# Kernel tuning notes

Measured on AMD Instinct MI355X. Metric: run time of the kernel, lower is better.

The kernel has to match this reference:

```python
import jax, jax.numpy as jnp
import numpy as np

B, N, D, H = 4, 2048, 1024, 16
HD = D // H
LR_SCALE = 0.01  # base step size for the fast-weight test-time update
EPS = 1e-6


def setup_inputs() -> dict:
    key = jax.random.key(0)
    ks = jax.random.split(key, 11)
    s = 0.02
    x = jax.random.normal(ks[0], (B, N, D), jnp.float32)
    Wq = jax.random.normal(ks[1], (D, D), jnp.float32) * s
    Wk = jax.random.normal(ks[2], (D, D), jnp.float32) * s
    Wv = jax.random.normal(ks[3], (D, D), jnp.float32) * s
    Wo = jax.random.normal(ks[4], (D, D), jnp.float32) * s
    w1_init = jax.random.normal(ks[5], (H, HD, HD), jnp.float32) * s  # FastWeightGLU init state
    w3_init = jax.random.normal(ks[6], (H, HD, HD), jnp.float32) * s
    W_lr = jax.random.normal(ks[7], (D, H), jnp.float32) * s  # FastWeightHpGLU lr head
    norm_w = jnp.ones((D,), jnp.float32)  # grouped RMSNorm weight
    Wg1 = jax.random.normal(ks[8], (D, HD), jnp.float32) * s  # output_gate bottleneck
    Wg2 = jax.random.normal(ks[9], (HD, D), jnp.float32) * s
    return dict(x=x, Wq=Wq, Wk=Wk, Wv=Wv, Wo=Wo, w1_init=w1_init,
                w3_init=w3_init, W_lr=W_lr, norm_w=norm_w, Wg1=Wg1, Wg2=Wg2)


def _fast_weight_train(q, k, v, lr, w1_init, w3_init):
    # q,k,v: (b,n,h,hd); lr: (b,n,h); fast weight f(x) = silu(x@W1) * (x@W3)
    b = q.shape[0]
    W1_0 = jnp.broadcast_to(w1_init, (b,) + w1_init.shape)
    W3_0 = jnp.broadcast_to(w3_init, (b,) + w3_init.shape)

    def step(carry, inp):
        W1, W3 = carry
        q_t, k_t, v_t, lr_t = inp  # (b,h,hd), lr_t: (b,h,1)
        h1 = jnp.einsum('bhd,bhde->bhe', k_t, W1)
        h3 = jnp.einsum('bhd,bhde->bhe', k_t, W3)
        sg = jax.nn.sigmoid(h1)
        s1 = h1 * sg  # silu(h1)
        err = s1 * h3 - v_t  # d(0.5||f(k)-v||^2)/df
        dsilu = sg * (1.0 + h1 * (1.0 - sg))
        g1 = err * h3 * dsilu
        g3 = err * s1
        W1 = W1 - lr_t[..., None] * jnp.einsum('bhd,bhe->bhde', k_t, g1)
        W3 = W3 - lr_t[..., None] * jnp.einsum('bhd,bhe->bhde', k_t, g3)
        o1 = jnp.einsum('bhd,bhde->bhe', q_t, W1)
        o3 = jnp.einsum('bhd,bhde->bhe', q_t, W3)
        return (W1, W3), jax.nn.silu(o1) * o3

    xs = (q.transpose(1, 0, 2, 3), k.transpose(1, 0, 2, 3),
          v.transpose(1, 0, 2, 3), lr.transpose(1, 0, 2)[..., None])
    (W1, W3), outs = jax.lax.scan(step, (W1_0, W3_0), xs)
    return outs.transpose(1, 0, 2, 3), (W1, W3)  # (b,n,h,hd)


def reference(x, Wq, Wk, Wv, Wo, w1_init, w3_init, W_lr, norm_w, Wg1, Wg2):
    b, n, d = x.shape
    h = w1_init.shape[0]
    hd = d // h
    q = jax.nn.silu((x @ Wq).reshape(b, n, h, hd))
    k = jax.nn.silu((x @ Wk).reshape(b, n, h, hd))
    v = (x @ Wv).reshape(b, n, h, hd)
    lr = LR_SCALE * jax.nn.sigmoid(x @ W_lr)  # (b,n,h) per-token hyper-param
    out, _ = _fast_weight_train(q, k, v, lr, w1_init, w3_init)
    # grouped RMSNorm (per head) fused with sigmoid output gate
    rms = jax.lax.rsqrt(jnp.mean(out * out, axis=-1, keepdims=True) + EPS)
    out = (out * rms).reshape(b, n, d) * norm_w
    gate = (x @ Wg1) @ Wg2
    out = out * jax.nn.sigmoid(gate)
    return out @ Wo
```

## Files before the change

### kernel.cpp

```cpp
#include <hip/hip_runtime.h>
#include <hip/hip_bf16.h>

#define B_ 4
#define N_ 2048
#define D_ 1024
#define H_ 16
#define HD_ 64
#define MTOT (B_*N_)
#define CH_ 16
#define NCH_ (N_/CH_)

typedef __attribute__((ext_vector_type(8))) short short8v;
typedef __attribute__((ext_vector_type(4))) float f32x4;

__device__ __forceinline__ float fsig(float x){
  return __builtin_amdgcn_rcpf(1.0f + __expf(-x));
}

__global__ void k_cast_bf16(const float* __restrict__ in, __hip_bfloat16* __restrict__ out, int n4){
  int i = blockIdx.x*256 + threadIdx.x;
  if (i >= n4) return;
  float4 vv = ((const float4*)in)[i];
  __hip_bfloat16 b0 = __float2bfloat16(vv.x), b1 = __float2bfloat16(vv.y),
                 b2 = __float2bfloat16(vv.z), b3 = __float2bfloat16(vv.w);
  ushort4 o;
  o.x = *(const unsigned short*)&b0; o.y = *(const unsigned short*)&b1;
  o.z = *(const unsigned short*)&b2; o.w = *(const unsigned short*)&b3;
  ((ushort4*)out)[i] = o;
}

__global__ void k_transpose_cast(const float* __restrict__ in, __hip_bfloat16* __restrict__ out,
                                 int R, int C){
  __shared__ float tile[64][65];
  int r0 = blockIdx.y*64, c0 = blockIdx.x*64;
  int tid = threadIdx.x;
  #pragma unroll
  for (int i=0;i<16;i++){ int idx = tid + i*256; int rr = idx>>6, cc = idx&63;
    tile[rr][cc] = in[(size_t)(r0+rr)*C + (c0+cc)]; }
  __syncthreads();
  #pragma unroll
  for (int i=0;i<16;i++){ int idx = tid + i*256; int rr = idx>>6, cc = idx&63;
    out[(size_t)(c0+rr)*R + (r0+cc)] = __float2bfloat16(tile[cc][rr]); }
}

__global__ void k_prep_wgl(const float* __restrict__ Wg1, const float* __restrict__ Wlr,
                           __hip_bfloat16* __restrict__ WgL){
  int idx = blockIdx.x*256 + threadIdx.x;
  int r = idx >> 10, d = idx & 1023;
  float v = 0.f;
  if (r < 64) v = Wg1[(size_t)d*64 + r];
  else if (r < 80) v = Wlr[(size_t)d*16 + (r-64)];
  WgL[idx] = __float2bfloat16(v);
}

__global__ void k_post_gl(const float* __restrict__ proj, __hip_bfloat16* __restrict__ t1,
                          float* __restrict__ lrout){
  int m = blockIdx.x*4 + (threadIdx.x>>6);
  int e = threadIdx.x & 63;
  float val = proj[(size_t)m*128 + e];
  t1[(size_t)m*64 + e] = __float2bfloat16(val);
  if (e < 16){
    float s = proj[(size_t)m*128 + 64 + e];
    lrout[(size_t)m*16 + e] = 0.01f*fsig(s);
  }
}

__device__ __forceinline__ void gl2lds16(const void* g, void* l){
  __builtin_amdgcn_global_load_lds((const __attribute__((address_space(1))) void*)g,
                                   (__attribute__((address_space(3))) void*)l, 16, 0, 0);
}

template<int ACT, int LAYOUT>
__global__ __launch_bounds__(256,2) void k_gemm_bt2(
    const __hip_bfloat16* __restrict__ A, const __hip_bfloat16* __restrict__ BT,
    float* __restrict__ C, int M, int N, int K)
{
  __shared__ short As[128*32];
  __shared__ short Bs[128*32];
  const int n0 = blockIdx.x*128, m0 = blockIdx.y*128;
  const int tid = threadIdx.x, lane = tid & 63, wid = tid >> 6;
  const int wm = wid >> 1, wn = wid & 1;
  const short* Aps = (const short*)A;
  const short* Bps = (const short*)BT;
  f32x4 acc[4][4] = {};
  const int srow = wid*32 + (lane>>2);
  const int scol = (lane&3)*8;
  const size_t aoff0 = (size_t)(m0+srow)*K + scol;
  const size_t boff0 = (size_t)(n0+srow)*K + scol;
  short* lA = As + wid*1024;
  short* lB = Bs + wid*1024;
  const int row = lane & 15, kq = (lane >> 4)*8;
  for (int kk = 0; kk < K; kk += 32) {
    __syncthreads();
    gl2lds16(Aps + aoff0 + kk,                 lA);
    gl2lds16(Aps + aoff0 + (size_t)16*K + kk,  lA + 512);
    gl2lds16(Bps + boff0 + kk,                 lB);
    gl2lds16(Bps + boff0 + (size_t)16*K + kk,  lB + 512);
    __syncthreads();
    short8v af[4], bfr[4];
    #pragma unroll
    for (int i=0;i<4;i++) af[i]  = *(const short8v*)(As + (wm*64 + i*16 + row)*32 + kq);
    #pragma unroll
    for (int j=0;j<4;j++) bfr[j] = *(const short8v*)(Bs + (wn*64 + j*16 + row)*32 + kq);
    #pragma unroll
    for (int i=0;i<4;i++)
      #pragma unroll
      for (int j=0;j<4;j++)
        acc[i][j] = __builtin_amdgcn_mfma_f32_16x16x32_bf16(af[i], bfr[j], acc[i][j], 0, 0, 0);
  }
  #pragma unroll
  for (int i=0;i<4;i++){
    #pragma unroll
    for (int j=0;j<4;j++){
      int col = n0 + wn*64 + j*16 + (lane & 15);
      #pragma unroll
      for (int qq=0; qq<4; ++qq){
        int rowg = m0 + wm*64 + i*16 + (lane>>4)*4 + qq;
        float val = acc[i][j][qq];
        if (ACT==1) val = val*fsig(val);
        if (LAYOUT==0) {
          C[(size_t)rowg*N + col] = val;
        } else {
          size_t oidx = ((((size_t)(rowg>>11))*16 + (col>>6))*(size_t)N_ + (size_t)(rowg & 2047))*64
                        + (size_t)(col & 63);
          C[oidx] = val;
        }
      }
    }
  }
}

__device__ __forceinline__ unsigned short bfr16(float x){
  __hip_bfloat16 b = __float2bfloat16(x);
  return *(unsigned short*)&b;
}
__device__ __forceinline__ short8v cvt_frag(const float4 a, const float4 c){
  short8v r;
  r[0]=(short)bfr16(a.x); r[1]=(short)bfr16(a.y); r[2]=(short)bfr16(a.z); r[3]=(short)bfr16(a.w);
  r[4]=(short)bfr16(c.x); r[5]=(short)bfr16(c.y); r[6]=(short)bfr16(c.z); r[7]=(short)bfr16(c.w);
  return r;
}

__global__ __launch_bounds__(256,1) void k_scan8(
    const float* __restrict__ q, const float* __restrict__ k, const float* __restrict__ v,
    const float* __restrict__ lr, const float* __restrict__ w1i, const float* __restrict__ w3i,
    float* __restrict__ so)
{
  const int blk = blockIdx.x;
  const int bh  = blk >> 2;
  const int sl  = blk & 3;
  const int b = bh >> 4, h = bh & 15;
  const int e0 = sl*16;
  const int tid = threadIdx.x, lane = tid & 63, wid = tid >> 6;
  const int tA = lane & 15, ks8 = (lane >> 4)*8;

  __shared__ __align__(16) __hip_bfloat16 Wb1[16*64];
  __shared__ __align__(16) __hip_bfloat16 Wb3[16*64];
  __shared__ __align__(16) float KW1e[256], KW3e[256];
  __shared__ __align__(16) float QW1[256], QW3[256];
  __shared__ __align__(16) float GKK[256], GQK[256];
  __shared__ __align__(16) float C13[512];

  const int we = tid & 15;
  const int wd = (tid >> 4) * 4;
  float w1r[4], w3r[4];
  {
    const float* w1p = w1i + (size_t)h*HD_*HD_ + e0 + we;
    const float* w3p = w3i + (size_t)h*HD_*HD_ + e0 + we;
    #pragma unroll
    for (int j=0;j<4;j++){ w1r[j] = w1p[(size_t)(wd+j)*64]; w3r[j] = w3p[(size_t)(wd+j)*64]; }
  }
  const int mir_off = we*128 + ((wd*2) ^ ((we&7)<<4));
  auto write_mirrors = [&](){
    uint2 p1, p3;
    p1.x = (unsigned)bfr16(w1r[0]) | ((unsigned)bfr16(w1r[1])<<16);
    p1.y = (unsigned)bfr16(w1r[2]) | ((unsigned)bfr16(w1r[3])<<16);
    p3.x = (unsigned)bfr16(w3r[0]) | ((unsigned)bfr16(w3r[1])<<16);
    p3.y = (unsigned)bfr16(w3r[2]) | ((unsigned)bfr16(w3r[3])<<16);
    *(uint2*)((char*)Wb1 + mir_off) = p1;
    *(uint2*)((char*)Wb3 + mir_off) = p3;
  };
  write_mirrors();

  const float* kfb = k + (size_t)bh*N_*64;
  const float* qfb = q + (size_t)bh*N_*64;
  const float* vfb = v + (size_t)bh*N_*64;
  const float* lrp = lr + ((size_t)b*N_)*16 + h;
  float* sob = so + (((size_t)b*N_)*16 + h)*64 + e0;

  auto mir_read = [&](const __hip_bfloat16* Wm, int m)->short8v{
    return *(const short8v*)((const char*)Wm + tA*128 + (((m*32+ks8)*2) ^ ((tA&7)<<4)));
  };

  float4 fA0,fA1,fA2,fA3;
  float4 fB0,fB1,fB2,fB3;
  float  vvr[16], lrr[16];

  if (wid >= 1) {
    const float* xr = ((wid==2) ? qfb : kfb) + (size_t)tA*64;
    fA0 = *(const float4*)(xr+ks8);    fA1 = *(const float4*)(xr+ks8+4);
    fA2 = *(const float4*)(xr+32+ks8); fA3 = *(const float4*)(xr+32+ks8+4);
    if (wid==3){
      const float* qr = qfb + (size_t)tA*64;
      fB0 = *(const float4*)(qr+ks8);    fB1 = *(const float4*)(qr+ks8+4);
      fB2 = *(const float4*)(qr+32+ks8); fB3 = *(const float4*)(qr+32+ks8+4);
    }
  } else if (lane < 16) {
    #pragma unroll
    for (int t=0;t<CH_;++t){
      vvr[t] = vfb[(size_t)t*64 + e0 + lane];
      lrr[t] = lrp[(size_t)t*16];
    }
  }
  __syncthreads();

  #pragma unroll 1
  for (int c = 0; c < NCH_; ++c) {
    const int t0 = c*CH_;

    if (wid == 1) {
      short8v af0 = cvt_frag(fA0,fA1), af1 = cvt_frag(fA2,fA3);
      const int slot = (((lane>>4)*4) ^ ((( tA>>1)&3)<<2));
      f32x4 acc = {};
      acc = __builtin_amdgcn_mfma_f32_16x16x32_bf16(af0, mir_read(Wb1,0), acc, 0,0,0);
      acc = __builtin_amdgcn_mfma_f32_16x16x32_bf16(af1, mir_read(Wb1,1), acc, 0,0,0);
      *(f32x4*)&KW1e[tA*16 + slot] = acc;
      f32x4 ac3 = {};
      ac3 = __builtin_amdgcn_mfma_f32_16x16x32_bf16(af0, mir_read(Wb3,0), ac3, 0,0,0);
      ac3 = __builtin_amdgcn_mfma_f32_16x16x32_bf16(af1, mir_read(Wb3,1), ac3, 0,0,0);
      *(f32x4*)&KW3e[tA*16 + slot] = ac3;
    } else if (wid == 2) {
      short8v af0 = cvt_frag(fA0,fA1), af1 = cvt_frag(fA2,fA3);
      f32x4 acc = {};
      acc = __builtin_amdgcn_mfma_f32_16x16x32_bf16(af0, mir_read(Wb1,0), acc, 0,0,0);
      acc = __builtin_amdgcn_mfma_f32_16x16x32_bf16(af1, mir_read(Wb1,1), acc, 0,0,0);
      #pragma unroll
      for (int qq=0;qq<4;++qq) QW1[((lane>>4)*4+qq)*16 + tA] = acc[qq];
      f32x4 ac3 = {};
      ac3 = __builtin_amdgcn_mfma_f32_16x16x32_bf16(af0, mir_read(Wb3,0), ac3, 0,0,0);
      ac3 = __builtin_amdgcn_mfma_f32_16x16x32_bf16(af1, mir_read(Wb3,1), ac3, 0,0,0);
      #pragma unroll
      for (int qq=0;qq<4;++qq) QW3[((lane>>4)*4+qq)*16 + tA] = ac3[qq];
    } else if (wid == 3) {
      short8v af0 = cvt_frag(fA0,fA1), af1 = cvt_frag(fA2,fA3);
      short8v aq0 = cvt_frag(fB0,fB1), aq1 = cvt_frag(fB2,fB3);
      f32x4 acc = {};
      acc = __builtin_amdgcn_mfma_f32_16x16x32_bf16(af0, af0, acc, 0,0,0);
      acc = __builtin_amdgcn_mfma_f32_16x16x32_bf16(af1, af1, acc, 0,0,0);
      #pragma unroll
      for (int qq=0;qq<4;++qq) GKK[((lane>>4)*4+qq)*16 + tA] = acc[qq];
      f32x4 ac2 = {};
      ac2 = __builtin_amdgcn_mfma_f32_16x16x32_bf16(aq0, af0, ac2, 0,0,0);
      ac2 = __builtin_amdgcn_mfma_f32_16x16x32_bf16(aq1, af1, ac2, 0,0,0);
      #pragma unroll
      for (int qq=0;qq<4;++qq) GQK[((lane>>4)*4+qq)*16 + tA] = ac2[qq];
    }
    __syncthreads();

    const int tn0 = ((c+1 < NCH_) ? c+1 : c) * CH_;
    if (wid >= 1) {
      const float* xr = ((wid==2) ? qfb : kfb) + (size_t)(tn0+tA)*64;
      fA0 = *(const float4*)(xr+ks8);    fA1 = *(const float4*)(xr+ks8+4);
      fA2 = *(const float4*)(xr+32+ks8); fA3 = *(const float4*)(xr+32+ks8+4);
      if (wid==3){
        const float* qr = qfb + (size_t)(tn0+tA)*64;
        fB0 = *(const float4*)(qr+ks8);    fB1 = *(const float4*)(qr+ks8+4);
        fB2 = *(const float4*)(qr+32+ks8); fB3 = *(const float4*)(qr+32+ks8+4);
      }
    } else if (lane < 16) {
      float vvn[16], lrn[16];
      #pragma unroll
      for (int t=0;t<CH_;++t){
        vvn[t] = vfb[(size_t)(tn0+t)*64 + e0 + lane];
        lrn[t] = lrp[(size_t)(tn0+t)*16];
      }
      float a1[16], a3[16];
      const int swr = ((lane>>1)&3)<<2;
      #pragma unroll
      for (int i2=0;i2<4;i2++){
        f32x4 x1 = *(const f32x4*)&KW1e[lane*16 + ((i2*4) ^ swr)];
        f32x4 x3 = *(const f32x4*)&KW3e[lane*16 + ((i2*4) ^ swr)];
        a1[i2*4+0]=x1[0]; a1[i2*4+1]=x1[1]; a1[i2*4+2]=x1[2]; a1[i2*4+3]=x1[3];
        a3[i2*4+0]=x3[0]; a3[i2*4+1]=x3[1]; a3[i2*4+2]=x3[2]; a3[i2*4+3]=x3[3];
      }
      f32x4 grow[3][4];
      #pragma unroll
      for (int i2=0;i2<4;i2++){
        grow[0][i2] = *(const f32x4*)&GKK[ 0 + i2*4];
        grow[1][i2] = *(const f32x4*)&GKK[16 + i2*4];
        grow[2][i2] = *(const f32x4*)&GKK[32 + i2*4];
      }
      #pragma unroll
      for (int t = 0; t < CH_; ++t) {
        const float h1 = a1[t], h3 = a3[t];
        const float sg = fsig(h1);
        const float s1 = h1*sg;
        const float er = fmaf(s1, h3, -vvr[t]);
        const float ds = sg*fmaf(h1, 1.0f - sg, 1.0f);
        const float lt = lrr[t];
        float2 cc; cc.x = lt*(er*h3*ds); cc.y = lt*(er*s1);
        *(float2*)&C13[(t*16+lane)*2] = cc;
        #pragma unroll
        for (int t2 = t+1; t2 < CH_; ++t2) {
          const float g = grow[t%3][t2>>2][t2&3];
          a1[t2] = fmaf(-g, cc.x, a1[t2]);
          a3[t2] = fmaf(-g, cc.y, a3[t2]);
        }
        if (t + 3 < CH_) {
          #pragma unroll
          for (int i2=0;i2<4;i2++) grow[(t+3)%3][i2] = *(const f32x4*)&GKK[(t+3)*16 + i2*4];
        }
      }
      #pragma unroll
      for (int t=0;t<CH_;++t){ vvr[t]=vvn[t]; lrr[t]=lrn[t]; }
    }
    __syncthreads();

    {
      const int ot = tid >> 4, oe = tid & 15;
      float o1 = QW1[ot*16+oe], o3 = QW3[ot*16+oe];
      #pragma unroll
      for (int s = 0; s < CH_; ++s) {
        const float gl2 = GQK[ot*16+s];
        const float2 cc = *(const float2*)&C13[(s*16+oe)*2];
        const float g = (s <= ot) ? gl2 : 0.0f;
        o1 = fmaf(-g, cc.x, o1);
        o3 = fmaf(-g, cc.y, o3);
      }
      sob[(size_t)(t0+ot)*(H_*HD_) + oe] = (o1*fsig(o1))*o3;
    }

    #pragma unroll
    for (int s = 0; s < CH_; ++s) {
      const float2 cc = *(const float2*)&C13[(s*16+we)*2];
      const float4 ks = *(const float4*)(kfb + (size_t)(t0+s)*64 + wd);
      w1r[0] = fmaf(-ks.x, cc.x, w1r[0]); w1r[1] = fmaf(-ks.y, cc.x, w1r[1]);
      w1r[2] = fmaf(-ks.z, cc.x, w1r[2]); w1r[3] = fmaf(-ks.w, cc.x, w1r[3]);
      w3r[0] = fmaf(-ks.x, cc.y, w3r[0]); w3r[1] = fmaf(-ks.y, cc.y, w3r[1]);
      w3r[2] = fmaf(-ks.z, cc.y, w3r[2]); w3r[3] = fmaf(-ks.w, cc.y, w3r[3]);
    }
    write_mirrors();
    __syncthreads();
  }
}

__global__ void k_norm_gate(const float* __restrict__ so, const float* __restrict__ gate,
                            const float* __restrict__ nw, __hip_bfloat16* __restrict__ y)
{
  int idx = blockIdx.x*4 + (threadIdx.x>>6);
  int e = threadIdx.x & 63;
  float o = so[(size_t)idx*64 + e];
  float ss = o*o;
  #pragma unroll
  for (int m=32; m>=1; m>>=1) ss += __shfl_xor(ss, m, 64);
  float rms = rsqrtf(ss*(1.0f/64.0f) + 1e-6f);
  int hh = idx & 15;
  size_t bn = (size_t)(idx >> 4);
  int d = hh*64 + e;
  float g = gate[bn*1024 + d];
  float val = o*rms*nw[d] * fsig(g);
  y[bn*1024 + d] = __float2bfloat16(val);
}

extern "C" void kernel_launch(void* const* d_in, const int* in_sizes, int n_in,
                              void* d_out, int out_size, void* d_ws, size_t ws_size,
                              hipStream_t stream)
{
  const float* x   = (const float*)d_in[0];
  const float* Wq  = (const float*)d_in[1];
  const float* Wk  = (const float*)d_in[2];
  const float* Wv  = (const float*)d_in[3];
  const float* Wo  = (const float*)d_in[4];
  const float* w1i = (const float*)d_in[5];
  const float* w3i = (const float*)d_in[6];
  const float* Wlr = (const float*)d_in[7];
  const float* nw  = (const float*)d_in[8];
  const float* Wg1 = (const float*)d_in[9];
  const float* Wg2 = (const float*)d_in[10];
  float* out = (float*)d_out;

  char* p = (char*)d_ws;
  auto take = [&](size_t bytes)->void*{ void* r = (void*)p; p += (bytes + 255) & ~(size_t)255; return r; };
  __hip_bfloat16* xb   = (__hip_bfloat16*)take((size_t)MTOT*D_*2);
  __hip_bfloat16* Wqt  = (__hip_bfloat16*)take((size_t)D_*D_*2);
  __hip_bfloat16* Wkt  = (__hip_bfloat16*)take((size_t)D_*D_*2);
  __hip_bfloat16* Wvt  = (__hip_bfloat16*)take((size_t)D_*D_*2);
  __hip_bfloat16* Wot  = (__hip_bfloat16*)take((size_t)D_*D_*2);
  __hip_bfloat16* Wg2t = (__hip_bfloat16*)take((size_t)D_*HD_*2);
  __hip_bfloat16* WgL  = (__hip_bfloat16*)take((size_t)128*D_*2);
  __hip_bfloat16* t1b  = (__hip_bfloat16*)take((size_t)MTOT*HD_*2);
  float* projt = (float*)take((size_t)MTOT*128*4);
  float* qf  = (float*)take((size_t)MTOT*D_*4);
  float* kf  = (float*)take((size_t)MTOT*D_*4);
  float* vf  = (float*)take((size_t)MTOT*D_*4);
  float* lrb = (float*)take((size_t)MTOT*H_*4);
  float* sob = (float*)take((size_t)MTOT*D_*4);
  __hip_bfloat16* yb = (__hip_bfloat16*)take((size_t)MTOT*D_*2);

  k_cast_bf16<<<MTOT*D_/4/256, 256, 0, stream>>>(x, xb, MTOT*D_/4);
  k_transpose_cast<<<dim3(16,16), 256, 0, stream>>>(Wq, Wqt, D_, D_);
  k_transpose_cast<<<dim3(16,16), 256, 0, stream>>>(Wk, Wkt, D_, D_);
  k_transpose_cast<<<dim3(16,16), 256, 0, stream>>>(Wv, Wvt, D_, D_);
  k_transpose_cast<<<dim3(16,16), 256, 0, stream>>>(Wo, Wot, D_, D_);
  k_transpose_cast<<<dim3(16,1),  256, 0, stream>>>(Wg2, Wg2t, HD_, D_);
  k_prep_wgl<<<512, 256, 0, stream>>>(Wg1, Wlr, WgL);
  k_gemm_bt2<0,0><<<dim3(1,64), 256, 0, stream>>>(xb, WgL, projt, MTOT, 128, D_);
  k_post_gl<<<MTOT/4, 256, 0, stream>>>(projt, t1b, lrb);
  k_gemm_bt2<1,1><<<dim3(8,64), 256, 0, stream>>>(xb, Wqt, qf, MTOT, D_, D_);
  k_gemm_bt2<1,1><<<dim3(8,64), 256, 0, stream>>>(xb, Wkt, kf, MTOT, D_, D_);
  k_gemm_bt2<0,1><<<dim3(8,64), 256, 0, stream>>>(xb, Wvt, vf, MTOT, D_, D_);
  k_gemm_bt2<0,0><<<dim3(8,64), 256, 0, stream>>>(t1b, Wg2t, out, MTOT, D_, HD_);
  k_scan8<<<256, 256, 0, stream>>>(qf, kf, vf, lrb, w1i, w3i, sob);
  k_norm_gate<<<MTOT*H_/4, 256, 0, stream>>>(sob, out, nw, yb);
  k_gemm_bt2<0,0><<<dim3(8,64), 256, 0, stream>>>(yb, Wot, out, MTOT, D_, D_);
}
```

Baseline: 558.8 us.

## Fuse Q/K/V projections into one GEMM and stage k chunk in LDS

The three separate Q, K and V projection GEMMs become a single GEMM over a concatenated transposed weight, with a new output layout mode that routes each third of the columns to the q, k or v buffer and applies SiLU only to the first two. The launch grid triples to 1536 blocks, which is meant to improve occupancy and cut launch overhead. Separately, the scan kernel now stores the k chunk it already loaded into a shared-memory tile and reads it from there for the fast-weight update, instead of re-reading k from global memory. This relies on qf, kf and vf being laid out contiguously in the workspace with no padding gap, which holds because each buffer's size is a multiple of 256 bytes.

```diff
diff --git a/kernel.cpp b/kernel.cpp
--- a/kernel.cpp
+++ b/kernel.cpp
@@ -117,12 +117,20 @@
       for (int qq=0; qq<4; ++qq){
         int rowg = m0 + wm*64 + i*16 + (lane>>4)*4 + qq;
         float val = acc[i][j][qq];
-        if (ACT==1) val = val*fsig(val);
         if (LAYOUT==0) {
+          if (ACT==1) val = val*fsig(val);
           C[(size_t)rowg*N + col] = val;
-        } else {
+        } else if (LAYOUT==1) {
+          if (ACT==1) val = val*fsig(val);
           size_t oidx = ((((size_t)(rowg>>11))*16 + (col>>6))*(size_t)N_ + (size_t)(rowg & 2047))*64
                         + (size_t)(col & 63);
+          C[oidx] = val;
+        } else {
+          const int t3 = col >> 10, cc2 = col & 1023;
+          if (t3 < 2) val = val*fsig(val);
+          size_t oidx = (size_t)t3*((size_t)MTOT*D_)
+                      + ((((size_t)(rowg>>11))*16 + (cc2>>6))*(size_t)N_ + (size_t)(rowg & 2047))*64
+                      + (size_t)(cc2 & 63);
           C[oidx] = val;
         }
       }
@@ -160,6 +168,7 @@
   __shared__ __align__(16) float QW1[256], QW3[256];
   __shared__ __align__(16) float GKK[256], GQK[256];
   __shared__ __align__(16) float C13[512];
+  __shared__ __align__(16) float kS[16][68];
 
   const int we = tid & 15;
   const int wd = (tid >> 4) * 4;
@@ -219,6 +228,10 @@
     const int t0 = c*CH_;
 
     if (wid == 1) {
+      *(float4*)&kS[tA][ks8]      = fA0;
+      *(float4*)&kS[tA][ks8+4]    = fA1;
+      *(float4*)&kS[tA][32+ks8]   = fA2;
+      *(float4*)&kS[tA][32+ks8+4] = fA3;
       short8v af0 = cvt_frag(fA0,fA1), af1 = cvt_frag(fA2,fA3);
       const int slot = (((lane>>4)*4) ^ ((( tA>>1)&3)<<2));
       f32x4 acc = {};
@@ -333,7 +346,7 @@
     #pragma unroll
     for (int s = 0; s < CH_; ++s) {
       const float2 cc = *(const float2*)&C13[(s*16+we)*2];
-      const float4 ks = *(const float4*)(kfb + (size_t)(t0+s)*64 + wd);
+      const float4 ks = *(const float4*)&kS[s][wd];
       w1r[0] = fmaf(-ks.x, cc.x, w1r[0]); w1r[1] = fmaf(-ks.y, cc.x, w1r[1]);
       w1r[2] = fmaf(-ks.z, cc.x, w1r[2]); w1r[3] = fmaf(-ks.w, cc.x, w1r[3]);
       w3r[0] = fmaf(-ks.x, cc.y, w3r[0]); w3r[1] = fmaf(-ks.y, cc.y, w3r[1]);
@@ -381,14 +394,12 @@
 
   char* p = (char*)d_ws;
   auto take = [&](size_t bytes)->void*{ void* r = (void*)p; p += (bytes + 255) & ~(size_t)255; return r; };
-  __hip_bfloat16* xb   = (__hip_bfloat16*)take((size_t)MTOT*D_*2);
-  __hip_bfloat16* Wqt  = (__hip_bfloat16*)take((size_t)D_*D_*2);
-  __hip_bfloat16* Wkt  = (__hip_bfloat16*)take((size_t)D_*D_*2);
-  __hip_bfloat16* Wvt  = (__hip_bfloat16*)take((size_t)D_*D_*2);
-  __hip_bfloat16* Wot  = (__hip_bfloat16*)take((size_t)D_*D_*2);
-  __hip_bfloat16* Wg2t = (__hip_bfloat16*)take((size_t)D_*HD_*2);
-  __hip_bfloat16* WgL  = (__hip_bfloat16*)take((size_t)128*D_*2);
-  __hip_bfloat16* t1b  = (__hip_bfloat16*)take((size_t)MTOT*HD_*2);
+  __hip_bfloat16* xb    = (__hip_bfloat16*)take((size_t)MTOT*D_*2);
+  __hip_bfloat16* WqkvT = (__hip_bfloat16*)take((size_t)3*D_*D_*2);
+  __hip_bfloat16* Wot   = (__hip_bfloat16*)take((size_t)D_*D_*2);
+  __hip_bfloat16* Wg2t  = (__hip_bfloat16*)take((size_t)D_*HD_*2);
+  __hip_bfloat16* WgL   = (__hip_bfloat16*)take((size_t)128*D_*2);
+  __hip_bfloat16* t1b   = (__hip_bfloat16*)take((size_t)MTOT*HD_*2);
   float* projt = (float*)take((size_t)MTOT*128*4);
   float* qf  = (float*)take((size_t)MTOT*D_*4);
   float* kf  = (float*)take((size_t)MTOT*D_*4);
@@ -396,19 +407,18 @@
   float* lrb = (float*)take((size_t)MTOT*H_*4);
   float* sob = (float*)take((size_t)MTOT*D_*4);
   __hip_bfloat16* yb = (__hip_bfloat16*)take((size_t)MTOT*D_*2);
+  (void)kf; (void)vf;
 
   k_cast_bf16<<<MTOT*D_/4/256, 256, 0, stream>>>(x, xb, MTOT*D_/4);
-  k_transpose_cast<<<dim3(16,16), 256, 0, stream>>>(Wq, Wqt, D_, D_);
-  k_transpose_cast<<<dim3(16,16), 256, 0, stream>>>(Wk, Wkt, D_, D_);
-  k_transpose_cast<<<dim3(16,16), 256, 0, stream>>>(Wv, Wvt, D_, D_);
+  k_transpose_cast<<<dim3(16,16), 256, 0, stream>>>(Wq, WqkvT,             D_, D_);
+  k_transpose_cast<<<dim3(16,16), 256, 0, stream>>>(Wk, WqkvT + D_*D_,     D_, D_);
+  k_transpose_cast<<<dim3(16,16), 256, 0, stream>>>(Wv, WqkvT + 2*D_*D_,   D_, D_);
   k_transpose_cast<<<dim3(16,16), 256, 0, stream>>>(Wo, Wot, D_, D_);
   k_transpose_cast<<<dim3(16,1),  256, 0, stream>>>(Wg2, Wg2t, HD_, D_);
   k_prep_wgl<<<512, 256, 0, stream>>>(Wg1, Wlr, WgL);
   k_gemm_bt2<0,0><<<dim3(1,64), 256, 0, stream>>>(xb, WgL, projt, MTOT, 128, D_);
   k_post_gl<<<MTOT/4, 256, 0, stream>>>(projt, t1b, lrb);
-  k_gemm_bt2<1,1><<<dim3(8,64), 256, 0, stream>>>(xb, Wqt, qf, MTOT, D_, D_);
-  k_gemm_bt2<1,1><<<dim3(8,64), 256, 0, stream>>>(xb, Wkt, kf, MTOT, D_, D_);
-  k_gemm_bt2<0,1><<<dim3(8,64), 256, 0, stream>>>(xb, Wvt, vf, MTOT, D_, D_);
+  k_gemm_bt2<1,2><<<dim3(24,64), 256, 0, stream>>>(xb, WqkvT, qf, MTOT, 3*D_, D_);
   k_gemm_bt2<0,0><<<dim3(8,64), 256, 0, stream>>>(t1b, Wg2t, out, MTOT, D_, HD_);
   k_scan8<<<256, 256, 0, stream>>>(qf, kf, vf, lrb, w1i, w3i, sob);
   k_norm_gate<<<MTOT*H_/4, 256, 0, stream>>>(sob, out, nw, yb);
```

New measurement: 524.6 us. -6.1%, faster.
